# Kernel optimization log

Hardware: AMD Instinct MI355X
Metric: run time of the kernel (lower is better)

The kernel has to match this reference:

```python
import jax, jax.numpy as jnp
import numpy as np

N, E, DIM, H = 50000, 800000, 64, 4

def setup_inputs() -> dict:
    key = jax.random.key(0)
    k0, k1, k2, k3, k4 = jax.random.split(key, 5)
    h_v = jax.random.normal(k0, (N, DIM), dtype=jnp.float32)
    src = jax.random.randint(k1, (E,), 0, N, dtype=jnp.int64)
    dst = jax.random.randint(k2, (E,), 0, N, dtype=jnp.int64)
    W_fc = jax.random.normal(k3, (DIM * H, DIM), dtype=jnp.float32) * 0.05
    b_fc = jnp.zeros((DIM * H,), dtype=jnp.float32)
    W_pi = jax.random.normal(k4, (1, DIM * H), dtype=jnp.float32) * 0.05
    return {"h_v": h_v, "src": src, "dst": dst, "W_fc": W_fc, "b_fc": b_fc, "W_pi": W_pi}

def reference(h_v, src, dst, W_fc, b_fc, W_pi):
    n, dim = h_v.shape
    heads = W_fc.shape[0] // dim
    # fc: [N, dim] -> [N, H*dim]
    ft = h_v @ W_fc.T + b_fc
    # u_mul_v: per-edge elementwise product of src/dst features  [E, H*dim]
    e = ft[src] * ft[dst]
    # pi + LeakyReLU(0.2): per-edge scalar score  [E]
    s = jax.nn.leaky_relu(e @ W_pi.T, negative_slope=0.2)[:, 0]
    # edge_softmax over incoming edges of each destination node (stable)
    smax = jax.ops.segment_max(s, dst, num_segments=n)
    ex = jnp.exp(s - smax[dst])
    denom = jax.ops.segment_sum(ex, dst, num_segments=n)
    a = ex / denom[dst]                        # [E]
    # u_mul_e + scatter-sum into destination nodes  [N, H*dim]
    agg = jax.ops.segment_sum(ft[src] * a[:, None], dst, num_segments=n)
    # max-pool over heads  [N, dim]
    return agg.reshape(n, heads, dim).max(axis=1)
```

## Files before the change

### kernel.cpp

```cpp
#include <hip/hip_runtime.h>
#include <math.h>

#define DIM 64
#define FDIM 256
#define MAXD 64
#define DEFER_THR 4.0f

typedef _Float16 h2 __attribute__((ext_vector_type(2)));
typedef float f2 __attribute__((ext_vector_type(2)));

__global__ __launch_bounds__(256) void fc_kernel(const float* __restrict__ h,
                                                 const float* __restrict__ W,
                                                 const float* __restrict__ b,
                                                 _Float16* __restrict__ ft,
                                                 int* __restrict__ cnt, int N)
{
    for (int i = blockIdx.x * blockDim.x + threadIdx.x; i < N;
         i += gridDim.x * blockDim.x) cnt[i] = 0;

    int t = threadIdx.x;
    float w[DIM];
#pragma unroll
    for (int j = 0; j < DIM / 4; ++j) {
        float4 v = *(const float4*)(W + (size_t)t * DIM + j * 4);
        w[4 * j + 0] = v.x; w[4 * j + 1] = v.y;
        w[4 * j + 2] = v.z; w[4 * j + 3] = v.w;
    }
    float bt = b[t];
    for (int r = blockIdx.x; r < N; r += gridDim.x) {
        const float4* h4 = (const float4*)(h + (size_t)r * DIM);
        float acc = bt;
#pragma unroll
        for (int j = 0; j < DIM / 4; ++j) {
            float4 hv = h4[j];
            acc = fmaf(hv.x, w[4 * j + 0], acc);
            acc = fmaf(hv.y, w[4 * j + 1], acc);
            acc = fmaf(hv.z, w[4 * j + 2], acc);
            acc = fmaf(hv.w, w[4 * j + 3], acc);
        }
        ft[(size_t)r * FDIM + t] = (_Float16)acc;
    }
}

__global__ void bucket_kernel(const int* __restrict__ src, const int* __restrict__ dst,
                              int* __restrict__ cnt, int* __restrict__ egrid, int E)
{
    int i = blockIdx.x * blockDim.x + threadIdx.x;
    if (i < E) {
        int d = dst[i];
        int slot = atomicAdd(&cnt[d], 1);
        egrid[(size_t)d * MAXD + slot] = src[i];
    }
}

__global__ __launch_bounds__(256) void agg_kernel(const _Float16* __restrict__ ft,
                                                  const int* __restrict__ cnt,
                                                  const int* __restrict__ egrid,
                                                  const float* __restrict__ Wpi,
                                                  float* __restrict__ out, int N)
{
    __shared__ float xb[4][1280];
    int wid = (blockIdx.x * blockDim.x + threadIdx.x) >> 6;
    int wv  = threadIdx.x >> 6;
    int lane = threadIdx.x & 63;
    if (wid >= N) return;
    int q  = lane >> 4;
    int ql = lane & 15;

    h2 fdwh[8];
    {
        const float* wp = Wpi + ql * 16;
        const _Float16* drow = ft + (size_t)wid * FDIM + ql * 16;
        uint4 a = *(const uint4*)(drow);
        uint4 b = *(const uint4*)(drow + 8);
        const h2* da = (const h2*)&a;
        const h2* db = (const h2*)&b;
#pragma unroll
        for (int j = 0; j < 4; ++j) {
            h2 v = da[j], u = db[j];
            fdwh[j].x     = (_Float16)((float)v.x * wp[2 * j + 0]);
            fdwh[j].y     = (_Float16)((float)v.y * wp[2 * j + 1]);
            fdwh[4 + j].x = (_Float16)((float)u.x * wp[8 + 2 * j + 0]);
            fdwh[4 + j].y = (_Float16)((float)u.y * wp[8 + 2 * j + 1]);
        }
    }

    int e0 = wid * MAXD;
    int e1 = e0 + cnt[wid];
    float mq = -INFINITY, lq = 0.f;
    f2 acc2[8];
#pragma unroll
    for (int j = 0; j < 8; ++j) acc2[j] = (f2){0.f, 0.f};

    auto LOAD8 = [&](uint4& a1, uint4& b1, uint4& a2, uint4& b2,
                     bool& v1, bool& v2, int bse) {
        int lo = bse + q, hi = bse + q + 4;
        v1 = lo < e1; v2 = hi < e1;
        int s1 = egrid[v1 ? lo : e0];
        int s2 = egrid[v2 ? hi : e0];
        const _Float16* r1 = ft + (size_t)s1 * FDIM + ql * 16;
        const _Float16* r2 = ft + (size_t)s2 * FDIM + ql * 16;
        a1 = *(const uint4*)(r1);
        b1 = *(const uint4*)(r1 + 8);
        a2 = *(const uint4*)(r2);
        b2 = *(const uint4*)(r2 + 8);
    };
    auto COMP8 = [&](uint4 a1, uint4 b1, uint4 a2, uint4 b2, bool v1, bool v2) {
        const h2* fa1 = (const h2*)&a1; const h2* fb1 = (const h2*)&b1;
        const h2* fa2 = (const h2*)&a2; const h2* fb2 = (const h2*)&b2;
        float p1 = 0.f, p2 = 0.f;
#pragma unroll
        for (int j = 0; j < 4; ++j) {
            p1 = __builtin_amdgcn_fdot2(fa1[j], fdwh[j], p1, false);
            p2 = __builtin_amdgcn_fdot2(fa2[j], fdwh[j], p2, false);
        }
#pragma unroll
        for (int j = 0; j < 4; ++j) {
            p1 = __builtin_amdgcn_fdot2(fb1[j], fdwh[4 + j], p1, false);
            p2 = __builtin_amdgcn_fdot2(fb2[j], fdwh[4 + j], p2, false);
        }
        p1 += __shfl_xor(p1, 1, 64);  p2 += __shfl_xor(p2, 1, 64);
        p1 += __shfl_xor(p1, 2, 64);  p2 += __shfl_xor(p2, 2, 64);
        p1 += __shfl_xor(p1, 4, 64);  p2 += __shfl_xor(p2, 4, 64);
        p1 += __shfl_xor(p1, 8, 64);  p2 += __shfl_xor(p2, 8, 64);
        float s1 = p1 > 0.f ? p1 : 0.2f * p1;
        float s2 = p2 > 0.f ? p2 : 0.2f * p2;
        if (!v1) s1 = -INFINITY;
        if (!v2) s2 = -INFINITY;
        float smax = fmaxf(s1, s2);
        if (smax > mq + DEFER_THR) {
            float sc = __expf(mq - smax);
            lq *= sc;
            f2 sc2 = {sc, sc};
#pragma unroll
            for (int j = 0; j < 8; ++j) acc2[j] *= sc2;
            mq = smax;
        }
        float pe1 = v1 ? __expf(s1 - mq) : 0.f;
        float pe2 = v2 ? __expf(s2 - mq) : 0.f;
        lq += pe1 + pe2;
        f2 pe1v = {pe1, pe1}, pe2v = {pe2, pe2};
#pragma unroll
        for (int j = 0; j < 4; ++j) {
            f2 w1 = {(float)fa1[j].x, (float)fa1[j].y};
            f2 w2 = {(float)fa2[j].x, (float)fa2[j].y};
            acc2[j] = __builtin_elementwise_fma(pe1v, w1,
                       __builtin_elementwise_fma(pe2v, w2, acc2[j]));
            f2 u1 = {(float)fb1[j].x, (float)fb1[j].y};
            f2 u2 = {(float)fb2[j].x, (float)fb2[j].y};
            acc2[4 + j] = __builtin_elementwise_fma(pe1v, u1,
                           __builtin_elementwise_fma(pe2v, u2, acc2[4 + j]));
        }
    };

    if (e0 < e1) {
        uint4 Aa1, Ab1, Aa2, Ab2, Ba1, Bb1, Ba2, Bb2;
        bool Av1, Av2, Bv1, Bv2;
        int base = e0;
        LOAD8(Aa1, Ab1, Aa2, Ab2, Av1, Av2, base);
        while (true) {
            int nxt = base + 8;
            bool more = nxt < e1;
            if (more) LOAD8(Ba1, Bb1, Ba2, Bb2, Bv1, Bv2, nxt);
            COMP8(Aa1, Ab1, Aa2, Ab2, Av1, Av2);
            if (!more) break;
            base = nxt;
            nxt = base + 8;
            more = nxt < e1;
            if (more) LOAD8(Aa1, Ab1, Aa2, Ab2, Av1, Av2, nxt);
            COMP8(Ba1, Bb1, Ba2, Bb2, Bv1, Bv2);
            if (!more) break;
            base = nxt;
        }
    }

    float mstar = fmaxf(mq, __shfl_xor(mq, 16, 64));
    mstar = fmaxf(mstar, __shfl_xor(mstar, 32, 64));
    float sc = (lq > 0.f) ? __expf(mq - mstar) : 0.f;
    float lt = lq * sc;
    lt += __shfl_xor(lt, 16, 64);
    lt += __shfl_xor(lt, 32, 64);
    float inv = (lt > 0.f) ? 1.f / lt : 0.f;

    {
        float* wp = &xb[wv][(unsigned)lane * 20];
        f2 sc2 = {sc, sc};
#pragma unroll
        for (int k = 0; k < 4; ++k) {
            f2 lo = acc2[2 * k] * sc2;
            f2 hi = acc2[2 * k + 1] * sc2;
            *(float4*)(wp + 4 * k) = make_float4(lo.x, lo.y, hi.x, hi.y);
        }
    }
    asm volatile("s_waitcnt lgkmcnt(0)" ::: "memory");
    {
        int col = lane >> 4, jp = lane & 15;
        float A[4];
#pragma unroll
        for (int h = 0; h < 4; ++h) {
            int rowb = (col + 4 * h) * 20 + jp;
            float v0 = xb[wv][rowb];
            float v1 = xb[wv][rowb + 16 * 20];
            float v2 = xb[wv][rowb + 32 * 20];
            float v3 = xb[wv][rowb + 48 * 20];
            A[h] = (v0 + v1) + (v2 + v3);
        }
        float r = fmaxf(fmaxf(A[0], A[1]), fmaxf(A[2], A[3])) * inv;
        out[(size_t)wid * DIM + lane] = r;
    }
}

extern "C" void kernel_launch(void* const* d_in, const int* in_sizes, int n_in,
                              void* d_out, int out_size, void* d_ws, size_t ws_size,
                              hipStream_t stream)
{
    const float* h_v  = (const float*)d_in[0];
    const int*   src  = (const int*)d_in[1];
    const int*   dst  = (const int*)d_in[2];
    const float* W_fc = (const float*)d_in[3];
    const float* b_fc = (const float*)d_in[4];
    const float* W_pi = (const float*)d_in[5];
    float* out = (float*)d_out;

    int N = in_sizes[0] / DIM;
    int E = in_sizes[1];

    _Float16* ft = (_Float16*)d_ws;
    size_t ftB = (((size_t)N * FDIM * 2) + 255) & ~(size_t)255;
    char*  p     = (char*)d_ws + ftB;
    int*   cnt   = (int*)(p);
    int*   egrid = (int*)(p + 256 * 1024);

    int eb = (E + 255) / 256;
    fc_kernel<<<1024, 256, 0, stream>>>(h_v, W_fc, b_fc, ft, cnt, N);
    bucket_kernel<<<eb, 256, 0, stream>>>(src, dst, cnt, egrid, E);
    int blocks = (N * 64 + 255) / 256;
    agg_kernel<<<blocks, 256, 0, stream>>>(ft, cnt, egrid, W_pi, out, N);
}
```

Before: 148.7 us.

## Store edge-bucket source indices as 16-bit and compute two FC rows per iteration

The per-destination bucket grid now stores source node indices as unsigned short instead of int. This halves the footprint of the scattered bucket writes and of the index reads in the aggregation kernel, but only works while N stays at or below 65536. Separately, the FC kernel now processes two rows per loop iteration, reusing the register-held weights and giving two independent FMA chains for more instruction-level parallelism. A tail loop handles an odd final row.

```diff
diff --git a/kernel.cpp b/kernel.cpp
--- a/kernel.cpp
+++ b/kernel.cpp
@@ -27,7 +27,29 @@
         w[4 * j + 2] = v.z; w[4 * j + 3] = v.w;
     }
     float bt = b[t];
-    for (int r = blockIdx.x; r < N; r += gridDim.x) {
+    int ng = N >> 1;
+    for (int g = blockIdx.x; g < ng; g += gridDim.x) {
+        int r0 = g * 2;
+        const float4* hA = (const float4*)(h + (size_t)r0 * DIM);
+        const float4* hB = hA + (DIM / 4);
+        float a0 = bt, a1 = bt;
+#pragma unroll
+        for (int j = 0; j < DIM / 4; ++j) {
+            float4 vA = hA[j];
+            float4 vB = hB[j];
+            a0 = fmaf(vA.x, w[4 * j + 0], a0);
+            a1 = fmaf(vB.x, w[4 * j + 0], a1);
+            a0 = fmaf(vA.y, w[4 * j + 1], a0);
+            a1 = fmaf(vB.y, w[4 * j + 1], a1);
+            a0 = fmaf(vA.z, w[4 * j + 2], a0);
+            a1 = fmaf(vB.z, w[4 * j + 2], a1);
+            a0 = fmaf(vA.w, w[4 * j + 3], a0);
+            a1 = fmaf(vB.w, w[4 * j + 3], a1);
+        }
+        ft[(size_t)r0 * FDIM + t]        = (_Float16)a0;
+        ft[(size_t)(r0 + 1) * FDIM + t]  = (_Float16)a1;
+    }
+    for (int r = (ng << 1) + blockIdx.x; r < N; r += gridDim.x) {
         const float4* h4 = (const float4*)(h + (size_t)r * DIM);
         float acc = bt;
 #pragma unroll
@@ -43,19 +65,20 @@
 }
 
 __global__ void bucket_kernel(const int* __restrict__ src, const int* __restrict__ dst,
-                              int* __restrict__ cnt, int* __restrict__ egrid, int E)
+                              int* __restrict__ cnt, unsigned short* __restrict__ egrid,
+                              int E)
 {
     int i = blockIdx.x * blockDim.x + threadIdx.x;
     if (i < E) {
         int d = dst[i];
         int slot = atomicAdd(&cnt[d], 1);
-        egrid[(size_t)d * MAXD + slot] = src[i];
+        egrid[(size_t)d * MAXD + slot] = (unsigned short)src[i];
     }
 }
 
 __global__ __launch_bounds__(256) void agg_kernel(const _Float16* __restrict__ ft,
                                                   const int* __restrict__ cnt,
-                                                  const int* __restrict__ egrid,
+                                                  const unsigned short* __restrict__ egrid,
                                                   const float* __restrict__ Wpi,
                                                   float* __restrict__ out, int N)
 {
@@ -229,7 +252,7 @@
     size_t ftB = (((size_t)N * FDIM * 2) + 255) & ~(size_t)255;
     char*  p     = (char*)d_ws + ftB;
     int*   cnt   = (int*)(p);
-    int*   egrid = (int*)(p + 256 * 1024);
+    unsigned short* egrid = (unsigned short*)(p + 256 * 1024);
 
     int eb = (E + 255) / 256;
     fc_kernel<<<1024, 256, 0, stream>>>(h_v, W_fc, b_fc, ft, cnt, N);
```

Result: slower. 160.9 us (+8.2%).
